# Kernel optimization log

Measured on AMD Instinct MI355X. Metric: run time of the kernel, lower is better.

## Reference

```python
import jax, jax.numpy as jnp
import numpy as np

PI = 3.141592653589793


def setup_inputs() -> dict:
    key = jax.random.key(0)
    k1, k2, k3, k4 = jax.random.split(key, 4)
    B, N, C, H, V = 4, 4096, 128, 8, 16
    inputs = jax.random.normal(k1, (B, N, C), dtype=jnp.float32)
    dist = jax.random.uniform(k2, (N, N), dtype=jnp.float32)
    r = jax.random.normal(k3, (H, 1, 1), dtype=jnp.float32)
    weight = jax.random.normal(k4, (H, C, V), dtype=jnp.float32)
    return {"inputs": inputs, "dist": dist, "r": r, "weight": weight, "locality": 64}


def reference(inputs, dist, r, weight, locality):
    # scaled_dist: (H, N, N) -- learnable bandwidth per head via tan/sin transform
    scaled = dist[None, :, :] * jnp.tan(0.25 * PI * (1.0 + jnp.sin(r)))
    # quantile-based local masking along last axis (linear interpolation,
    # matching tfp.stats.percentile with interpolation='linear')
    mask = jnp.percentile(scaled, float(locality), axis=-1, keepdims=True, method="linear")
    fmax = jnp.finfo(jnp.float32).max
    scaled = jnp.where(scaled <= mask, scaled, fmax)
    # softmax over key axis of -scaled_dist (masked entries -> -fmax -> ~0 weight)
    att = jax.nn.softmax(-scaled, axis=-1)  # (H, N, N)
    # per-head value projection: (B,N,C) x (H,C,V) -> (B,H,N,V)
    value = jnp.einsum("bnj,hjk->bhnk", inputs, weight)
    # attention aggregation: (H,N,N) x (B,H,N,V) -> (B,H,N,V)
    concat = jnp.einsum("hnj,bhjd->bhnd", att, value)
    B, H, N, V = concat.shape
    concat = concat.transpose(0, 2, 1, 3).reshape(B, N, H * V)  # (B, N, hid_dim)
    # tf.keras.activations.gelu defaults to exact (non-approximate) gelu
    return jax.nn.gelu(concat, approximate=False)
```

## Files before the change

kernel.cpp:

```cpp
#include <hip/hip_runtime.h>
#include <hip/hip_bf16.h>
#include <math.h>

#define NN 4096
#define NC 128
#define NH 8
#define NV 16
#define NB 4
#define BD 64

typedef _Float16 half8 __attribute__((ext_vector_type(8)));
typedef __fp16  fp16x2 __attribute__((ext_vector_type(2)));
typedef float floatx4 __attribute__((ext_vector_type(4)));

__device__ __forceinline__ int get_loc(const int* locp){
    int lr = locp[0];
    return (lr >= 0 && lr <= 100) ? lr : 64;
}
__device__ __forceinline__ float head_scale(const float* rr, int h){
    float ts = tanf(0.78539816339744831f * (1.0f + sinf(rr[h])));
    if (!(ts > 0.f)) ts = (ts == 0.f) ? 1e-20f : 1e20f;
    if (ts > 1e20f) ts = 1e20f;
    return ts;
}
__device__ __forceinline__ void lds_barrier(){
    __asm__ __volatile__("s_waitcnt lgkmcnt(0)\n\ts_barrier" ::: "memory");
}

__global__ __launch_bounds__(256) void k_prep(const float* __restrict__ dist,
                                              const int* __restrict__ locp,
                                              const float* __restrict__ in,
                                              const float* __restrict__ wgt,
                                              float* __restrict__ Kval,
                                              float* __restrict__ xminp,
                                              _Float16* __restrict__ val_t){
    __shared__ unsigned int hist[4][256];
    __shared__ float cand[1024];
    __shared__ unsigned int cnt, selb_s, basec_s, xminu;

    const int t = threadIdx.x, lane = t & 63, wv = t >> 6;

    if (blockIdx.x < 512){
        const int idx = blockIdx.x;
        const int b   = idx & 3;
        const int j0  = (idx >> 2) * 32;
        const int kl  = (lane >> 4) * 8;
        const int v   = lane & 15;

        half8 Bf[2][4];
#pragma unroll
        for (int nt = 0; nt < 2; nt++){
            const int h = wv * 2 + nt;
            const float* wp = wgt + ((size_t)h * NC + kl) * NV + v;
#pragma unroll
            for (int kc = 0; kc < 4; kc++)
#pragma unroll
                for (int u = 0; u < 8; u++)
                    Bf[nt][kc][u] = (_Float16)wp[(kc * 32 + u) * NV];
        }

        floatx4 acc[2][2];
#pragma unroll
        for (int a = 0; a < 2; a++)
#pragma unroll
            for (int c = 0; c < 2; c++) acc[a][c] = (floatx4){0.f,0.f,0.f,0.f};

        const float* ip = in + ((size_t)b * NN + j0 + v) * NC + kl;
#pragma unroll
        for (int jm = 0; jm < 2; jm++){
            const float* ipm = ip + jm * 16 * NC;
#pragma unroll
            for (int kc = 0; kc < 4; kc++){
                float4 x0 = *(const float4*)(ipm + kc * 32);
                float4 x1 = *(const float4*)(ipm + kc * 32 + 4);
                const float xs[8] = {x0.x,x0.y,x0.z,x0.w,x1.x,x1.y,x1.z,x1.w};
                union { half8 h8; fp16x2 h2[4]; } hi, lo;
#pragma unroll
                for (int u = 0; u < 4; u++){
                    hi.h2[u] = __builtin_amdgcn_cvt_pkrtz(xs[2*u], xs[2*u+1]);
                    float r0 = xs[2*u]   - (float)hi.h2[u][0];
                    float r1 = xs[2*u+1] - (float)hi.h2[u][1];
                    lo.h2[u] = __builtin_amdgcn_cvt_pkrtz(r0, r1);
                }
#pragma unroll
                for (int nt = 0; nt < 2; nt++){
                    acc[jm][nt] = __builtin_amdgcn_mfma_f32_16x16x32_f16(hi.h8, Bf[nt][kc], acc[jm][nt], 0, 0, 0);
                    acc[jm][nt] = __builtin_amdgcn_mfma_f32_16x16x32_f16(lo.h8, Bf[nt][kc], acc[jm][nt], 0, 0, 0);
                }
            }
        }

        const int jw = (lane >> 4) * 4;
#pragma unroll
        for (int jm = 0; jm < 2; jm++)
#pragma unroll
            for (int nt = 0; nt < 2; nt++){
                const int h   = wv * 2 + nt;
                const int row = h * BD + b * NV + v;
                union { _Float16 hh[4]; uint2 u; } o;
#pragma unroll
                for (int u = 0; u < 4; u++) o.hh[u] = (_Float16)acc[jm][nt][u];
                *(uint2*)&val_t[(size_t)row * NN + j0 + jm * 16 + jw] = o.u;
            }
        return;
    }

    const int i = blockIdx.x - 512;
    const int loc = get_loc(locp);
    const unsigned int rank = (unsigned int)(((long long)loc * (NN - 1)) / 100) + 1u;

    float v[16];
    const float4* rp = (const float4*)(dist + (size_t)i * NN);
#pragma unroll
    for (int k = 0; k < 4; k++){
        float4 x4 = rp[k * 256 + t];
        v[4*k+0] = x4.x; v[4*k+1] = x4.y; v[4*k+2] = x4.z; v[4*k+3] = x4.w;
    }
    for (int k = t; k < 1024; k += 256) ((unsigned int*)hist)[k] = 0;
    if (t == 0){ cnt = 0; selb_s = 255u; basec_s = 0u; xminu = 0xFFFFFFFFu; }
    __syncthreads();

    float lmin = 1e30f;
#pragma unroll
    for (int u = 0; u < 16; u++){
        float x = v[u];
        lmin = fminf(lmin, x);
        int b = (int)(x * 256.0f); b = b < 0 ? 0 : (b > 255 ? 255 : b);
        atomicAdd(&hist[wv][b], 1u);
    }
#pragma unroll
    for (int off = 1; off < 64; off <<= 1) lmin = fminf(lmin, __shfl_xor(lmin, off));
    if (lane == 0) atomicMin(&xminu, __float_as_uint(lmin));
    __syncthreads();

    if (t < 64){
        unsigned int lp[4];
        unsigned int run = 0;
#pragma unroll
        for (int q = 0; q < 4; q++){
            int b = 4 * t + q;
            run += hist[0][b] + hist[1][b] + hist[2][b] + hist[3][b];
            lp[q] = run;
        }
        unsigned int incl = run;
#pragma unroll
        for (int d = 1; d < 64; d <<= 1){
            unsigned int y = __shfl_up(incl, d);
            if (t >= d) incl += y;
        }
        unsigned int excl = incl - run;
        if (excl < rank && rank <= incl){
#pragma unroll
            for (int q = 0; q < 4; q++){
                if (excl + lp[q] >= rank){
                    selb_s  = (unsigned int)(4 * t + q);
                    basec_s = excl + (q ? lp[q-1] : 0u);
                    break;
                }
            }
        }
    }
    __syncthreads();
    const unsigned int sb = selb_s;
    if (t == 0) Kval[i] = ((float)sb + 1.0f) * 0.00390625f;
#pragma unroll
    for (int u = 0; u < 16; u++){
        float x = v[u];
        int b = (int)(x * 256.0f); b = b < 0 ? 0 : (b > 255 ? 255 : b);
        if ((unsigned int)b == sb){
            unsigned int idx = atomicAdd(&cnt, 1u);
            if (idx < 1024u) cand[idx] = x;
        }
    }
    __syncthreads();
    const unsigned int n = cnt > 1024u ? 1024u : cnt;
    const unsigned int need = rank - basec_s;
    for (unsigned int c0 = t; c0 < n; c0 += 256){
        float x = cand[c0];
        unsigned int lt = 0, le = 0;
        for (unsigned int k2 = 0; k2 < n; k2++){
            float y = cand[k2];
            lt += (y < x); le += (y <= x);
        }
        if (lt < need && need <= le) Kval[i] = x;
    }
    if (t == 0) xminp[i] = __uint_as_float(xminu);
}

__global__ __launch_bounds__(512) void k_att(const float* __restrict__ dist,
                                             const float* __restrict__ rr,
                                             const _Float16* __restrict__ val_t,
                                             const float* __restrict__ Kvalp,
                                             const float* __restrict__ xminp,
                                             float* __restrict__ out){
    __shared__ alignas(16) _Float16 wtile[2][64 * 72];
    __shared__ alignas(16) _Float16 vtile[2][64 * 72];

    const int l   = blockIdx.x;
    const int xcd = l & 7;
    const int s   = l >> 3;
    const int i0  = (xcd * 8 + (s >> 3)) * 64;
    const int h   = s & 7;

    const int t = threadIdx.x;
    const int lane = t & 63, wv = t >> 6;
    const float ts  = head_scale(rr, h);
    const float ts2 = ts * 1.44269504088896f;
    const float nts2 = -ts2;

    const int il = t >> 3, jq = t & 7;
    const float kvi  = Kvalp[i0 + il];
    const float txmi = ts2 * xminp[i0 + il];

    const float* dp = dist + (size_t)(i0 + il) * NN + jq * 8;
    const _Float16* vp = val_t + (size_t)(h * BD + il) * NN + jq * 8;

    half8 ones;
#pragma unroll
    for (int u = 0; u < 8; u++) ones[u] = (_Float16)1.0f;

    floatx4 acc0 = (floatx4){0.f,0.f,0.f,0.f};
    floatx4 acc1 = (floatx4){0.f,0.f,0.f,0.f};
    floatx4 accs = (floatx4){0.f,0.f,0.f,0.f};

    const int iq16 = (wv >> 1) * 16;
    const int bh   = (wv & 1) * 32;
    const int aoff  = (iq16 + (lane & 15)) * 72 + (lane >> 4) * 8;
    const int boff0 = (bh + (lane & 15)) * 72 + (lane >> 4) * 8;
    const int boff1 = boff0 + 16 * 72;
    const int voff  = il * 72 + jq * 8;
    const int woff  = voff;

    uint4  Av, Bv;
    float4 Ad0, Ad1, Bd0, Bd1;

#define LOADSET(V, D0, D1) do{                                               \
        V  = *(const uint4*)vp;  vp += 64;                                   \
        D0 = *(const float4*)dp;                                             \
        D1 = *(const float4*)(dp + 4);  dp += 64; }while(0)

#define STAGE(BUF, V, D0, D1) do{                                            \
        *(uint4*)&vtile[BUF][voff] = V;                                      \
        const float dd_[8] = {D0.x,D0.y,D0.z,D0.w,D1.x,D1.y,D1.z,D1.w};      \
        union { half8 h8; fp16x2 h2[4]; } uu_;                               \
        _Pragma("unroll")                                                    \
        for (int u_ = 0; u_ < 4; u_++){                                      \
            float a0_ = fmaf(nts2, dd_[2*u_  ], txmi);                       \
            float a1_ = fmaf(nts2, dd_[2*u_+1], txmi);                       \
            a0_ = (dd_[2*u_  ] <= kvi) ? a0_ : -20000.0f;                    \
            a1_ = (dd_[2*u_+1] <= kvi) ? a1_ : -20000.0f;                    \
            uu_.h2[u_] = __builtin_amdgcn_cvt_pkrtz(                         \
                __builtin_amdgcn_exp2f(a0_), __builtin_amdgcn_exp2f(a1_));   \
        }                                                                    \
        *(half8*)&wtile[BUF][woff] = uu_.h8; }while(0)

#define MFMA_T(BUF) do{                                                      \
        _Pragma("unroll")                                                    \
        for (int kc_ = 0; kc_ < 2; kc_++){                                   \
            half8 af = *(const half8*)&wtile[BUF][aoff  + kc_ * 32];         \
            half8 b0 = *(const half8*)&vtile[BUF][boff0 + kc_ * 32];         \
            half8 b1 = *(const half8*)&vtile[BUF][boff1 + kc_ * 32];         \
            acc0 = __builtin_amdgcn_mfma_f32_16x16x32_f16(af, b0, acc0, 0, 0, 0); \
            acc1 = __builtin_amdgcn_mfma_f32_16x16x32_f16(af, b1, acc1, 0, 0, 0); \
            accs = __builtin_amdgcn_mfma_f32_16x16x32_f16(af, ones, accs, 0, 0, 0); \
        } }while(0)

    LOADSET(Av, Ad0, Ad1);
    LOADSET(Bv, Bd0, Bd1);
    STAGE(0, Av, Ad0, Ad1);

    for (int jp = 0; jp < 31; jp++){
        LOADSET(Av, Ad0, Ad1);
        lds_barrier();
        MFMA_T(0);
        STAGE(1, Bv, Bd0, Bd1);
        LOADSET(Bv, Bd0, Bd1);
        lds_barrier();
        MFMA_T(1);
        STAGE(0, Av, Ad0, Ad1);
    }
    lds_barrier();
    MFMA_T(0);
    STAGE(1, Bv, Bd0, Bd1);
    lds_barrier();
    MFMA_T(1);

#undef LOADSET
#undef STAGE
#undef MFMA_T

    const int m0 = (lane >> 4) * 4;
    const int d  = lane & 15;
#pragma unroll
    for (int r4 = 0; r4 < 4; r4++){
        const int i = i0 + iq16 + m0 + r4;
        const float inv_s = 1.0f / fmaxf(accs[r4], 1e-30f);
#pragma unroll
        for (int nt = 0; nt < 2; nt++){
            const int b = (wv & 1) * 2 + nt;
            float c = acc0[r4], c1 = acc1[r4];
            float cc = (nt == 0 ? c : c1) * inv_s;
            float g = 0.5f * cc * (1.0f + erff(cc * 0.70710678118654752f));
            out[((size_t)b * NN + i) * (NH * NV) + h * NV + d] = g;
        }
    }
}

extern "C" void kernel_launch(void* const* d_in, const int* in_sizes, int n_in,
                              void* d_out, int out_size, void* d_ws, size_t ws_size,
                              hipStream_t stream) {
    const float* in   = (const float*)d_in[0];
    const float* dist = (const float*)d_in[1];
    const float* r    = (const float*)d_in[2];
    const float* wgt  = (const float*)d_in[3];
    const int*   loc  = (const int*)d_in[4];
    float* out = (float*)d_out;

    float* Kval = (float*)d_ws;
    float* xmin = Kval + NN;
    _Float16* val_t = (_Float16*)((char*)d_ws + 2 * (size_t)NN * sizeof(float));

    k_prep<<<512 + NN, 256, 0, stream>>>(dist, loc, in, wgt, Kval, xmin, val_t);
    k_att<<<512, 512, 0, stream>>>(dist, r, val_t, Kval, xmin, out);
}
```

Before: 158.7 us.

## Use 2x2 MFMA register tiles with K-split waves and XOR-swizzled LDS

Reorganizes the attention MFMA inner loop so each wave computes a 32x32 output tile over half the K chunk. Each A and B fragment loaded from LDS is now reused twice, which cuts LDS reads per MFMA. Padded LDS rows (stride 72) are replaced by an XOR swizzle on a stride-64 layout to avoid bank conflicts. The two K-half partial sums are then reduced through LDS in the epilogue, which adds an extra barrier round and more accumulator registers.

```diff
diff --git a/kernel.cpp b/kernel.cpp
--- a/kernel.cpp
+++ b/kernel.cpp
@@ -193,14 +193,16 @@
                                              const float* __restrict__ Kvalp,
                                              const float* __restrict__ xminp,
                                              float* __restrict__ out){
-    __shared__ alignas(16) _Float16 wtile[2][64 * 72];
-    __shared__ alignas(16) _Float16 vtile[2][64 * 72];
-
-    const int l   = blockIdx.x;
-    const int xcd = l & 7;
-    const int s   = l >> 3;
-    const int i0  = (xcd * 8 + (s >> 3)) * 64;
-    const int h   = s & 7;
+    __shared__ alignas(16) char lds_raw[32768];
+    _Float16* wtile = (_Float16*)lds_raw;
+    _Float16* vtile = (_Float16*)(lds_raw + 16384);
+    float*    mrg   = (float*)lds_raw;
+
+    const int l    = blockIdx.x;
+    const int xcd  = l & 7;
+    const int sblk = l >> 3;
+    const int i0   = (xcd * 8 + (sblk >> 3)) * 64;
+    const int h    = sblk & 7;
 
     const int t = threadIdx.x;
     const int lane = t & 63, wv = t >> 6;
@@ -215,21 +217,29 @@
     const float* dp = dist + (size_t)(i0 + il) * NN + jq * 8;
     const _Float16* vp = val_t + (size_t)(h * BD + il) * NN + jq * 8;
 
+    const int stg = il * 64 + ((jq * 8) ^ ((il & 7) << 3));
+
+    const int sub   = wv >> 1;
+    const int khalf = wv & 1;
+    const int ih32  = (sub >> 1) * 32;
+    const int bh32  = (sub & 1) * 32;
+    const int cf    = khalf * 32 + (lane >> 4) * 8;
+    const int cswz  = (lane & 7) << 3;
+    const int aoff0 = (ih32 +      (lane & 15)) * 64 + (cf ^ cswz);
+    const int aoff1 = (ih32 + 16 + (lane & 15)) * 64 + (cf ^ cswz);
+    const int boff0 = (bh32 +      (lane & 15)) * 64 + (cf ^ cswz);
+    const int boff1 = (bh32 + 16 + (lane & 15)) * 64 + (cf ^ cswz);
+
     half8 ones;
 #pragma unroll
     for (int u = 0; u < 8; u++) ones[u] = (_Float16)1.0f;
 
-    floatx4 acc0 = (floatx4){0.f,0.f,0.f,0.f};
-    floatx4 acc1 = (floatx4){0.f,0.f,0.f,0.f};
-    floatx4 accs = (floatx4){0.f,0.f,0.f,0.f};
-
-    const int iq16 = (wv >> 1) * 16;
-    const int bh   = (wv & 1) * 32;
-    const int aoff  = (iq16 + (lane & 15)) * 72 + (lane >> 4) * 8;
-    const int boff0 = (bh + (lane & 15)) * 72 + (lane >> 4) * 8;
-    const int boff1 = boff0 + 16 * 72;
-    const int voff  = il * 72 + jq * 8;
-    const int woff  = voff;
+    floatx4 acc00 = (floatx4){0.f,0.f,0.f,0.f};
+    floatx4 acc01 = (floatx4){0.f,0.f,0.f,0.f};
+    floatx4 acc10 = (floatx4){0.f,0.f,0.f,0.f};
+    floatx4 acc11 = (floatx4){0.f,0.f,0.f,0.f};
+    floatx4 accs0 = (floatx4){0.f,0.f,0.f,0.f};
+    floatx4 accs1 = (floatx4){0.f,0.f,0.f,0.f};
 
     uint4  Av, Bv;
     float4 Ad0, Ad1, Bd0, Bd1;
@@ -240,7 +250,7 @@
         D1 = *(const float4*)(dp + 4);  dp += 64; }while(0)
 
 #define STAGE(BUF, V, D0, D1) do{                                            \
-        *(uint4*)&vtile[BUF][voff] = V;                                      \
+        *(uint4*)&vtile[(BUF) * 4096 + stg] = V;                             \
         const float dd_[8] = {D0.x,D0.y,D0.z,D0.w,D1.x,D1.y,D1.z,D1.w};      \
         union { half8 h8; fp16x2 h2[4]; } uu_;                               \
         _Pragma("unroll")                                                    \
@@ -252,18 +262,21 @@
             uu_.h2[u_] = __builtin_amdgcn_cvt_pkrtz(                         \
                 __builtin_amdgcn_exp2f(a0_), __builtin_amdgcn_exp2f(a1_));   \
         }                                                                    \
-        *(half8*)&wtile[BUF][woff] = uu_.h8; }while(0)
+        *(half8*)&wtile[(BUF) * 4096 + stg] = uu_.h8; }while(0)
 
 #define MFMA_T(BUF) do{                                                      \
-        _Pragma("unroll")                                                    \
-        for (int kc_ = 0; kc_ < 2; kc_++){                                   \
-            half8 af = *(const half8*)&wtile[BUF][aoff  + kc_ * 32];         \
-            half8 b0 = *(const half8*)&vtile[BUF][boff0 + kc_ * 32];         \
-            half8 b1 = *(const half8*)&vtile[BUF][boff1 + kc_ * 32];         \
-            acc0 = __builtin_amdgcn_mfma_f32_16x16x32_f16(af, b0, acc0, 0, 0, 0); \
-            acc1 = __builtin_amdgcn_mfma_f32_16x16x32_f16(af, b1, acc1, 0, 0, 0); \
-            accs = __builtin_amdgcn_mfma_f32_16x16x32_f16(af, ones, accs, 0, 0, 0); \
-        } }while(0)
+        const int bb_ = (BUF) * 4096;                                        \
+        half8 a0 = *(const half8*)&wtile[bb_ + aoff0];                       \
+        half8 a1 = *(const half8*)&wtile[bb_ + aoff1];                       \
+        half8 b0 = *(const half8*)&vtile[bb_ + boff0];                       \
+        half8 b1 = *(const half8*)&vtile[bb_ + boff1];                       \
+        acc00 = __builtin_amdgcn_mfma_f32_16x16x32_f16(a0, b0, acc00, 0, 0, 0); \
+        acc01 = __builtin_amdgcn_mfma_f32_16x16x32_f16(a0, b1, acc01, 0, 0, 0); \
+        acc10 = __builtin_amdgcn_mfma_f32_16x16x32_f16(a1, b0, acc10, 0, 0, 0); \
+        acc11 = __builtin_amdgcn_mfma_f32_16x16x32_f16(a1, b1, acc11, 0, 0, 0); \
+        accs0 = __builtin_amdgcn_mfma_f32_16x16x32_f16(a0, ones, accs0, 0, 0, 0); \
+        accs1 = __builtin_amdgcn_mfma_f32_16x16x32_f16(a1, ones, accs1, 0, 0, 0); \
+        }while(0)
 
     LOADSET(Av, Ad0, Ad1);
     LOADSET(Bv, Bd0, Bd1);
@@ -289,17 +302,39 @@
 #undef STAGE
 #undef MFMA_T
 
-    const int m0 = (lane >> 4) * 4;
-    const int d  = lane & 15;
+    lds_barrier();
+    {
+        floatx4 w0, w1, w2;
+        if (khalf == 0){ w0 = acc10; w1 = acc11; w2 = accs1; }
+        else           { w0 = acc00; w1 = acc01; w2 = accs0; }
+        const int mb = wv * 768 + lane * 12;
+        *(floatx4*)&mrg[mb    ] = w0;
+        *(floatx4*)&mrg[mb + 4] = w1;
+        *(floatx4*)&mrg[mb + 8] = w2;
+    }
+    lds_barrier();
+    {
+        const int mb = (wv ^ 1) * 768 + lane * 12;
+        floatx4 m0 = *(const floatx4*)&mrg[mb    ];
+        floatx4 m1 = *(const floatx4*)&mrg[mb + 4];
+        floatx4 m2 = *(const floatx4*)&mrg[mb + 8];
+        if (khalf == 0){ acc00 += m0; acc01 += m1; accs0 += m2; }
+        else           { acc10 += m0; acc11 += m1; accs1 += m2; }
+    }
+
+    const floatx4 A0 = (khalf == 0) ? acc00 : acc10;
+    const floatx4 A1 = (khalf == 0) ? acc01 : acc11;
+    const floatx4 S  = (khalf == 0) ? accs0 : accs1;
+    const int m0i = (lane >> 4) * 4;
+    const int d   = lane & 15;
 #pragma unroll
     for (int r4 = 0; r4 < 4; r4++){
-        const int i = i0 + iq16 + m0 + r4;
-        const float inv_s = 1.0f / fmaxf(accs[r4], 1e-30f);
-#pragma unroll
-        for (int nt = 0; nt < 2; nt++){
-            const int b = (wv & 1) * 2 + nt;
-            float c = acc0[r4], c1 = acc1[r4];
-            float cc = (nt == 0 ? c : c1) * inv_s;
+        const int i = i0 + ih32 + khalf * 16 + m0i + r4;
+        const float inv_s = 1.0f / fmaxf(S[r4], 1e-30f);
+#pragma unroll
+        for (int bq = 0; bq < 2; bq++){
+            const int b = (sub & 1) * 2 + bq;
+            float cc = (bq == 0 ? A0[r4] : A1[r4]) * inv_s;
             float g = 0.5f * cc * (1.0f + erff(cc * 0.70710678118654752f));
             out[((size_t)b * NN + i) * (NH * NV) + h * NV + d] = g;
         }
```

Result: faster. 155.0 us (-2.3%).
